# Optimization experiments

Hardware: AMD Instinct MI355X
Metric: run time of the kernel (lower is better)

The kernel has to match this reference:

```python
import jax, jax.numpy as jnp
import numpy as np

M = 64      # bs_antenna_num
K = 16      # user_num
POWER = 1.0 # power_constr
B = 32768   # batch


def setup_inputs() -> dict:
    key = jax.random.key(0)
    P = jax.random.normal(key, (B, 2 * M * K), dtype=jnp.float32)
    return {"P": P}


def reference(P):
    b = P.shape[0]
    # recombine_P: per sample, real/imag halves each reshaped to (M, K)
    R = P[:, : M * K].reshape(b, M, K)   # real part, [B, M, K]
    I = P[:, M * K :].reshape(b, M, K)   # imag part, [B, M, K]
    # normalize_P (faithful to source): batch_size is overwritten by shape[0]
    # of the (M, K, B) tensor, i.e. it loops over ANTENNAS. Each antenna slice
    # temp = C[a, :, :] (K x B) is scaled so trace(temp @ temp^H) = POWER.
    # trace(temp @ conj(temp).T) = sum |temp|^2 = Frobenius energy, real > 0,
    # so the complex sqrt reduces to a real scale.
    energy = jnp.sum(R * R + I * I, axis=(0, 2))          # [M], per-antenna energy
    scale = jnp.sqrt(POWER / energy)                      # [M]
    Rn = R * scale[None, :, None]
    In = I * scale[None, :, None]
    # recover_P: flatten (M, K) row-major back into real|imag halves
    return jnp.concatenate([Rn.reshape(b, M * K), In.reshape(b, M * K)], axis=-1)
```

## Files before the change

kernel.cpp:

```cpp
#include <hip/hip_runtime.h>

#define M_ANT 64
#define POWER_CONSTR 1.0f

typedef float f32x4 __attribute__((ext_vector_type(4)));

__global__ __launch_bounds__(256) void energy_partial(
    const f32x4* __restrict__ P4, float* __restrict__ partials, int nvec) {
  const int tid = threadIdx.x;
  const int gtid = blockIdx.x * 256 + tid;
  const int stride = gridDim.x * 256;

  float acc = 0.0f;
  int f = gtid;
  for (; f + 3 * stride < nvec; f += 4 * stride) {
    f32x4 a = P4[f];
    f32x4 b = P4[f + stride];
    f32x4 c = P4[f + 2 * stride];
    f32x4 d = P4[f + 3 * stride];
    acc += a.x * a.x + a.y * a.y + a.z * a.z + a.w * a.w;
    acc += b.x * b.x + b.y * b.y + b.z * b.z + b.w * b.w;
    acc += c.x * c.x + c.y * c.y + c.z * c.z + c.w * c.w;
    acc += d.x * d.x + d.y * d.y + d.z * d.z + d.w * d.w;
  }
  for (; f < nvec; f += stride) {
    f32x4 v = P4[f];
    acc += v.x * v.x + v.y * v.y + v.z * v.z + v.w * v.w;
  }

  __shared__ float part[256];
  part[tid] = acc;
  __syncthreads();
  if (tid < 64) {
    float s = (part[4 * tid] + part[4 * tid + 1]) +
              (part[4 * tid + 2] + part[4 * tid + 3]);
    partials[blockIdx.x * 64 + tid] = s;
  }
}

__global__ __launch_bounds__(1024) void energy_finalize(
    const float* __restrict__ partials, float* __restrict__ scale, int nblocks) {
  const int tid = threadIdx.x;
  const int a = tid & 63;
  const int j = tid >> 6;
  float s = 0.0f;
  for (int b = j; b < nblocks; b += 16) s += partials[b * 64 + a];
  __shared__ float part[1024];
  part[tid] = s;
  __syncthreads();
  if (tid < 512) part[tid] += part[tid + 512];
  __syncthreads();
  if (tid < 256) part[tid] += part[tid + 256];
  __syncthreads();
  if (tid < 128) part[tid] += part[tid + 128];
  __syncthreads();
  if (tid < 64) {
    const float energy = part[tid] + part[tid + 64];
    scale[tid] = sqrtf(POWER_CONSTR / energy);
  }
}

__global__ __launch_bounds__(256) void apply_scale(
    const f32x4* __restrict__ P4, const float* __restrict__ scale,
    f32x4* __restrict__ O4, int nvec) {
  __shared__ float s_scale[M_ANT];
  if (threadIdx.x < M_ANT) s_scale[threadIdx.x] = scale[threadIdx.x];
  __syncthreads();

  const int gtid = blockIdx.x * 256 + threadIdx.x;
  const int stride = gridDim.x * 256;
  const float sc = s_scale[(threadIdx.x >> 2) & 63];

  if (gtid < nvec) {
    int k = (nvec - 1 - gtid) / stride;
    for (; k >= 0; --k) {
      const int f = gtid + k * stride;
      f32x4 v = __builtin_nontemporal_load(&P4[f]);
      v *= sc;
      __builtin_nontemporal_store(v, &O4[f]);
    }
  }
}

extern "C" void kernel_launch(void* const* d_in, const int* in_sizes, int n_in,
                              void* d_out, int out_size, void* d_ws, size_t ws_size,
                              hipStream_t stream) {
  const f32x4* P4 = (const f32x4*)d_in[0];
  f32x4* O4 = (f32x4*)d_out;
  float* ws = (float*)d_ws;

  const int nelem = in_sizes[0];
  const int nvec = nelem / 4;

  int nblocks1 = 2048;
  const size_t ws_floats = ws_size / sizeof(float);
  if (ws_floats < (size_t)nblocks1 * 64 + 64) {
    size_t cap = ws_floats > 64 ? (ws_floats - 64) / 64 : 1;
    nblocks1 = (int)(cap < 1 ? 1 : cap);
  }
  if (nblocks1 > (nvec + 255) / 256) nblocks1 = (nvec + 255) / 256;

  float* partials = ws;
  float* scale = ws + (size_t)nblocks1 * 64;

  energy_partial<<<nblocks1, 256, 0, stream>>>(P4, partials, nvec);
  energy_finalize<<<1, 1024, 0, stream>>>(partials, scale, nblocks1);

  int nblocks3 = (nvec + 255) / 256;
  if (nblocks3 > 2048) nblocks3 = 2048;
  apply_scale<<<nblocks3, 256, 0, stream>>>(P4, scale, O4, nvec);
}
```

Measured before the change: 168.7 us.

## Fuse energy finalize into partial kernel via last-block ticket reduction

Drops the separate single-block finalize kernel. Each block of the partial-energy pass takes an atomic ticket after a threadfence, and the last block to arrive reduces all partials and writes the per-antenna scales. The first pass also switches its loads to nontemporal. The ticket is reset with a hipMemsetAsync, so one kernel launch is replaced by a memset node, and the final reduction now runs on 256 threads instead of 1024.

```diff
diff --git a/kernel.cpp b/kernel.cpp
--- a/kernel.cpp
+++ b/kernel.cpp
@@ -6,7 +6,9 @@
 typedef float f32x4 __attribute__((ext_vector_type(4)));
 
 __global__ __launch_bounds__(256) void energy_partial(
-    const f32x4* __restrict__ P4, float* __restrict__ partials, int nvec) {
+    const f32x4* __restrict__ P4, float* __restrict__ partials,
+    float* __restrict__ scale, unsigned* __restrict__ ticket,
+    int nvec, int nblocks) {
   const int tid = threadIdx.x;
   const int gtid = blockIdx.x * 256 + tid;
   const int stride = gridDim.x * 256;
@@ -14,17 +16,17 @@
   float acc = 0.0f;
   int f = gtid;
   for (; f + 3 * stride < nvec; f += 4 * stride) {
-    f32x4 a = P4[f];
-    f32x4 b = P4[f + stride];
-    f32x4 c = P4[f + 2 * stride];
-    f32x4 d = P4[f + 3 * stride];
+    f32x4 a = __builtin_nontemporal_load(&P4[f]);
+    f32x4 b = __builtin_nontemporal_load(&P4[f + stride]);
+    f32x4 c = __builtin_nontemporal_load(&P4[f + 2 * stride]);
+    f32x4 d = __builtin_nontemporal_load(&P4[f + 3 * stride]);
     acc += a.x * a.x + a.y * a.y + a.z * a.z + a.w * a.w;
     acc += b.x * b.x + b.y * b.y + b.z * b.z + b.w * b.w;
     acc += c.x * c.x + c.y * c.y + c.z * c.z + c.w * c.w;
     acc += d.x * d.x + d.y * d.y + d.z * d.z + d.w * d.w;
   }
   for (; f < nvec; f += stride) {
-    f32x4 v = P4[f];
+    f32x4 v = __builtin_nontemporal_load(&P4[f]);
     acc += v.x * v.x + v.y * v.y + v.z * v.z + v.w * v.w;
   }
 
@@ -36,27 +38,29 @@
               (part[4 * tid + 2] + part[4 * tid + 3]);
     partials[blockIdx.x * 64 + tid] = s;
   }
-}
 
-__global__ __launch_bounds__(1024) void energy_finalize(
-    const float* __restrict__ partials, float* __restrict__ scale, int nblocks) {
-  const int tid = threadIdx.x;
-  const int a = tid & 63;
-  const int j = tid >> 6;
-  float s = 0.0f;
-  for (int b = j; b < nblocks; b += 16) s += partials[b * 64 + a];
-  __shared__ float part[1024];
-  part[tid] = s;
+  __threadfence();
+  __shared__ unsigned is_last;
+  if (tid == 0) {
+    unsigned t = atomicAdd(ticket, 1u);
+    is_last = (t == (unsigned)(nblocks - 1)) ? 1u : 0u;
+  }
   __syncthreads();
-  if (tid < 512) part[tid] += part[tid + 512];
-  __syncthreads();
-  if (tid < 256) part[tid] += part[tid + 256];
-  __syncthreads();
-  if (tid < 128) part[tid] += part[tid + 128];
-  __syncthreads();
-  if (tid < 64) {
-    const float energy = part[tid] + part[tid + 64];
-    scale[tid] = sqrtf(POWER_CONSTR / energy);
+  if (is_last) {
+    __threadfence();
+    const int a = tid & 63;
+    const int j = tid >> 6;
+    float s = 0.0f;
+    for (int b = j; b < nblocks; b += 4) s += partials[b * 64 + a];
+    __shared__ float p2[256];
+    p2[tid] = s;
+    __syncthreads();
+    if (tid < 128) p2[tid] += p2[tid + 128];
+    __syncthreads();
+    if (tid < 64) {
+      const float energy = p2[tid] + p2[tid + 64];
+      scale[tid] = sqrtf(POWER_CONSTR / energy);
+    }
   }
 }
 
@@ -94,17 +98,20 @@
 
   int nblocks1 = 2048;
   const size_t ws_floats = ws_size / sizeof(float);
-  if (ws_floats < (size_t)nblocks1 * 64 + 64) {
-    size_t cap = ws_floats > 64 ? (ws_floats - 64) / 64 : 1;
+  if (ws_floats < (size_t)nblocks1 * 64 + 65) {
+    size_t cap = ws_floats > 65 ? (ws_floats - 65) / 64 : 1;
     nblocks1 = (int)(cap < 1 ? 1 : cap);
   }
   if (nblocks1 > (nvec + 255) / 256) nblocks1 = (nvec + 255) / 256;
 
   float* partials = ws;
   float* scale = ws + (size_t)nblocks1 * 64;
+  unsigned* ticket = (unsigned*)(scale + 64);
 
-  energy_partial<<<nblocks1, 256, 0, stream>>>(P4, partials, nvec);
-  energy_finalize<<<1, 1024, 0, stream>>>(partials, scale, nblocks1);
+  hipMemsetAsync(ticket, 0, sizeof(unsigned), stream);
+
+  energy_partial<<<nblocks1, 256, 0, stream>>>(P4, partials, scale, ticket,
+                                               nvec, nblocks1);
 
   int nblocks3 = (nvec + 255) / 256;
   if (nblocks3 > 2048) nblocks3 = 2048;
```

After: 597.3 us. +254.1%, slower.
